# Kernel optimization log

Measured on AMD Instinct MI355X. Metric: run time of the kernel, lower is better.

Reference implementation:

```python
import jax, jax.numpy as jnp
import numpy as np

NUM_HEADS = 16
HIDDEN = 1024
HEAD_DIM = HIDDEN // NUM_HEADS
LN_EPS = 1e-5


def setup_inputs() -> dict:
    key = jax.random.key(0)
    ks = jax.random.split(key, 10)
    B, S, D = 2, 2048, HIDDEN
    std = 1.0 / np.sqrt(D)
    inp = {
        "hidden_states": jax.random.normal(ks[0], (B, S, D), dtype=jnp.float32),
        "attention_mask": jnp.zeros((B, 1, 1, S), dtype=jnp.float32),
        "Wq": jax.random.normal(ks[1], (D, D), dtype=jnp.float32) * std,
        "bq": jnp.zeros((D,), dtype=jnp.float32),
        "Wk": jax.random.normal(ks[2], (D, D), dtype=jnp.float32) * std,
        "bk": jnp.zeros((D,), dtype=jnp.float32),
        "Wv": jax.random.normal(ks[3], (D, D), dtype=jnp.float32) * std,
        "bv": jnp.zeros((D,), dtype=jnp.float32),
        "Wo": jax.random.normal(ks[4], (D, D), dtype=jnp.float32) * std,
        "bo": jnpp if False else jnp.zeros((D,), dtype=jnp.float32),
        "ln_gamma": jnp.ones((D,), dtype=jnp.float32),
        "ln_beta": jnp.zeros((D,), dtype=jnp.float32),
    }
    return inp


def _mha(x, mask, Wq, bq, Wk, bk, Wv, bv, Wo, bo, ln_gamma, ln_beta):
    B, S, D = x.shape
    H, Hd = NUM_HEADS, HEAD_DIM
    scale = 1.0 / np.sqrt(Hd).astype(np.float32)

    def split_heads(t):  # [B,S,D] -> [B,H,S,Hd]
        return t.reshape(B, S, H, Hd).transpose(0, 2, 1, 3)

    q = split_heads(x @ Wq + bq)
    k = split_heads(x @ Wk + bk)
    v = split_heads(x @ Wv + bv)

    scores = jnp.einsum("bhqd,bhkd->bhqk", q, k) * scale + mask
    probs = jax.nn.softmax(scores, axis=-1)
    ctx = jnp.einsum("bhqk,bhkd->bhqd", probs, v)
    ctx = ctx.transpose(0, 2, 1, 3).reshape(B, S, D)

    out = ctx @ Wo + bo
    resid = out + x
    mu = jnp.mean(resid, axis=-1, keepdims=True)
    var = jnp.var(resid, axis=-1, keepdims=True)
    return (resid - mu) * jax.lax.rsqrt(var + LN_EPS) * ln_gamma + ln_beta


def reference(hidden_states, attention_mask, Wq, bq, Wk, bk, Wv, bv, Wo, bo, ln_gamma, ln_beta):
    return _mha(hidden_states, attention_mask, Wq, bq, Wk, bk, Wv, bv, Wo, bo, ln_gamma, ln_beta)
```

## Files before the change

kernel.cpp:

```cpp
#include <hip/hip_runtime.h>
#include <hip/hip_bf16.h>
#include <stdint.h>

#define NUMH 16
#define HD   64
#define HID  1024
#define SEQ  2048
#define BATCH 2
#define NTOK (BATCH*SEQ)
#define LN_EPS 1e-5f

typedef __attribute__((ext_vector_type(8)))  short  short8;
typedef __attribute__((ext_vector_type(4)))  float  f32x4;
typedef __attribute__((ext_vector_type(16))) float  f32x16;

#define AS1 __attribute__((address_space(1)))
#define AS3 __attribute__((address_space(3)))

__device__ __forceinline__ void gload_lds16(const void* g, void* l) {
  __builtin_amdgcn_global_load_lds((const AS1 void*)g, (AS3 void*)l, 16, 0, 0);
}

__device__ __forceinline__ unsigned short f2bf(float f) {
  union { float f; unsigned u; } v; v.f = f;
  unsigned u = v.u;
  u += 0x7fffu + ((u >> 16) & 1u);
  return (unsigned short)(u >> 16);
}

__device__ __forceinline__ f32x4 mfma16x16x32(short8 a, short8 b, f32x4 c) {
  return __builtin_amdgcn_mfma_f32_16x16x32_bf16(a, b, c, 0, 0, 0);
}
__device__ __forceinline__ f32x16 mfma32x32x16(short8 a, short8 b, f32x16 c) {
  return __builtin_amdgcn_mfma_f32_32x32x16_bf16(a, b, c, 0, 0, 0);
}

__device__ __forceinline__ unsigned cvtpk(float lo, float hi) {
  unsigned r;
  asm("v_cvt_pk_bf16_f32 %0, %1, %2" : "=v"(r) : "v"(lo), "v"(hi));
  return r;
}
__device__ __forceinline__ void perm32swap(unsigned &a, unsigned &b) {
  asm volatile("v_permlane32_swap_b32 %0, %1" : "+v"(a), "+v"(b));
}
__device__ __forceinline__ float xhalf_max(float x) {
  union { float f; unsigned u; } a, b; a.f = x; b.f = x;
  perm32swap(a.u, b.u);
  return fmaxf(a.f, b.f);
}
__device__ __forceinline__ float xhalf_sum(float x) {
  union { float f; unsigned u; } a, b; a.f = x; b.f = x;
  perm32swap(a.u, b.u);
  return a.f + b.f;
}

__global__ void k_conv_x(const float* __restrict__ x, unsigned short* __restrict__ xb) {
  int i = blockIdx.x * blockDim.x + threadIdx.x;
  f32x4 v = ((const f32x4*)x)[i];
  unsigned short* o = xb + i * 4;
  o[0] = f2bf(v[0]); o[1] = f2bf(v[1]); o[2] = f2bf(v[2]); o[3] = f2bf(v[3]);
}

__global__ void k_transw_all(const float* __restrict__ Wq, const float* __restrict__ Wk,
                             const float* __restrict__ Wv, const float* __restrict__ Wo,
                             unsigned short* __restrict__ WqkvT, unsigned short* __restrict__ WoT) {
  __shared__ float t[32][33];
  int z = blockIdx.z;
  const float* in = (z == 0) ? Wq : (z == 1) ? Wk : (z == 2) ? Wv : Wo;
  unsigned short* out = (z < 3) ? WqkvT + (size_t)z * HID * HID : WoT;
  int tx = threadIdx.x, ty = threadIdx.y;
  int x0 = blockIdx.x * 32, y0 = blockIdx.y * 32;
  for (int j = 0; j < 32; j += 8)
    t[ty + j][tx] = in[(y0 + ty + j) * HID + x0 + tx];
  __syncthreads();
  for (int j = 0; j < 32; j += 8)
    out[(x0 + ty + j) * HID + y0 + tx] = f2bf(t[tx][ty + j]);
}

template<int MODE>
__global__ __launch_bounds__(256, 2)
void k_gemm(const unsigned short* __restrict__ A, const unsigned short* __restrict__ BT,
            int M, int N, int K,
            const float* __restrict__ bias0, const float* __restrict__ bias1,
            const float* __restrict__ bias2, const float* __restrict__ resid,
            unsigned short* __restrict__ outQ, unsigned short* __restrict__ outK,
            unsigned short* __restrict__ outV, float* __restrict__ outF) {
  const int tid  = threadIdx.x;
  const int lane = tid & 63, wave = tid >> 6;
  const int l15 = lane & 15, lhi = lane >> 4;
  const int row0 = blockIdx.x * 128, col0 = blockIdx.y * 128;
  const int wrow = (wave >> 1) * 64, wcol = (wave & 1) * 64;

  __shared__ unsigned short As[128 * 32];
  __shared__ unsigned short Bs[128 * 32];

  f32x4 acc[4][4] = {};

  for (int kt = 0; kt < K; kt += 32) {
    #pragma unroll
    for (int c = 0; c < 2; ++c) {
      int base = wave * 1024 + c * 4096;
      int o = base + lane * 16;
      int r = o >> 6, cb = o & 63;
      gload_lds16(A  + (size_t)(row0 + r) * K + kt + (cb >> 1), As + (base >> 1));
      gload_lds16(BT + (size_t)(col0 + r) * K + kt + (cb >> 1), Bs + (base >> 1));
    }
    __syncthreads();

    short8 af[4], bf[4];
    #pragma unroll
    for (int m = 0; m < 4; ++m)
      af[m] = *(const short8*)(As + (wrow + m * 16 + l15) * 32 + lhi * 8);
    #pragma unroll
    for (int n = 0; n < 4; ++n)
      bf[n] = *(const short8*)(Bs + (wcol + n * 16 + l15) * 32 + lhi * 8);
    #pragma unroll
    for (int m = 0; m < 4; ++m)
      #pragma unroll
      for (int n = 0; n < 4; ++n)
        acc[m][n] = mfma16x16x32(af[m], bf[n], acc[m][n]);
    __syncthreads();
  }

  #pragma unroll
  for (int m = 0; m < 4; ++m)
    #pragma unroll
    for (int n = 0; n < 4; ++n) {
      int col = col0 + wcol + n * 16 + l15;
      #pragma unroll
      for (int j = 0; j < 4; ++j) {
        int row = row0 + wrow + m * 16 + lhi * 4 + j;
        float v = acc[m][n][j];
        if (MODE == 0) {
          int proj = col >> 10, d = col & 1023;
          int h = d >> 6, hd = d & 63;
          int b = row >> 11, s = row & 2047;
          const float* bias = (proj == 0) ? bias0 : (proj == 1) ? bias1 : bias2;
          unsigned short* dst = (proj == 0) ? outQ : (proj == 1) ? outK : outV;
          dst[((size_t)((b * NUMH + h) * SEQ + s) << 6) + hd] = f2bf(v + bias[d]);
        } else {
          size_t idx = (size_t)row * N + col;
          outF[idx] = v + bias0[col] + resid[idx];
        }
      }
    }
}

__global__ void k_vtrans(const unsigned short* __restrict__ V, unsigned short* __restrict__ VT) {
  __shared__ unsigned short t[64][65];
  int bh = blockIdx.y, s0 = blockIdx.x * 64;
  int tid = threadIdx.x;
  for (int it = 0; it < 16; ++it) {
    int idx = it * 256 + tid;
    int r = idx >> 6, c = idx & 63;
    t[r][c] = V[(size_t)(bh * SEQ + s0 + r) * 64 + c];
  }
  __syncthreads();
  for (int it = 0; it < 16; ++it) {
    int idx = it * 256 + tid;
    int d = idx >> 6, sl = idx & 63;
    VT[(size_t)(bh * 64 + d) * SEQ + s0 + sl] = t[sl][d];
  }
}

__global__ __launch_bounds__(256, 2)
void k_attn(const unsigned short* __restrict__ Q, const unsigned short* __restrict__ Kk,
            const unsigned short* __restrict__ VT, const float* __restrict__ mask,
            unsigned short* __restrict__ ctx) {
  const int tid = threadIdx.x, lane = tid & 63, wave = tid >> 6;
  const int l31 = lane & 31, hi = lane >> 5;
  const int bh = blockIdx.x, b = bh >> 4, h = bh & 15;
  const int qs = blockIdx.y * 128 + wave * 32;

  __shared__ __align__(16) unsigned short Ks[2][64 * 64];
  __shared__ __align__(16) unsigned short Vs[2][64 * 64];
  __shared__ __align__(16) float sLds[4][32];

  short8 qf[4];
  {
    const unsigned short* qrow = Q + ((size_t)bh * SEQ + qs + l31) * 64 + hi * 8;
    #pragma unroll
    for (int ks = 0; ks < 4; ++ks) qf[ks] = *(const short8*)(qrow + ks * 16);
  }

  f32x16 o0 = {}, o1 = {};
  float mr = -3.0e38f, lr = 0.f;
  const float LOG2E = 1.44269504088896340736f;
  const float scale = 0.125f;
  const int sw = (l31 & 7) << 4;

  auto stage = [&](int bufi, int kt) {
    #pragma unroll
    for (int c = 0; c < 2; ++c) {
      int base = wave * 1024 + c * 4096;
      int off = base + lane * 16;
      int r = off >> 7, cb = off & 127;
      int scb = cb ^ ((r & 7) << 4);
      gload_lds16(Kk + ((size_t)bh * SEQ + kt + r) * 64 + (scb >> 1), &Ks[bufi][base >> 1]);
      gload_lds16(VT + ((size_t)bh * 64 + r) * SEQ + kt + (scb >> 1), &Vs[bufi][base >> 1]);
    }
  };

  stage(0, 0);
  __syncthreads();
  int cur = 0;

  for (int kt = 0; kt < SEQ; kt += 64) {
    if (kt + 64 < SEQ) stage(cur ^ 1, kt + 64);

    const unsigned short* Kc = Ks[cur];
    const unsigned short* Vc = Vs[cur];
    f32x16 s0 = {}, s1 = {};
    #pragma unroll
    for (int ks = 0; ks < 4; ++ks) {
      int cb = ((ks * 16 + hi * 8) * 2) ^ sw;
      short8 k0 = *(const short8*)((const char*)Kc + l31 * 128 + cb);
      short8 k1 = *(const short8*)((const char*)Kc + (32 + l31) * 128 + cb);
      s0 = mfma32x32x16(k0, qf[ks], s0);
      s1 = mfma32x32x16(k1, qf[ks], s1);
    }

    f32x4 mk0[4], mk1[4];
    #pragma unroll
    for (int rq = 0; rq < 4; ++rq) {
      mk0[rq] = *(const f32x4*)(mask + b * SEQ + kt + rq * 8 + hi * 4);
      mk1[rq] = *(const f32x4*)(mask + b * SEQ + kt + 32 + rq * 8 + hi * 4);
    }
    #pragma unroll
    for (int r = 0; r < 16; ++r) {
      s0[r] = fmaf(s0[r], scale, mk0[r >> 2][r & 3]);
      s1[r] = fmaf(s1[r], scale, mk1[r >> 2][r & 3]);
    }

    float tmax = fmaxf(s0[0], s1[0]);
    #pragma unroll
    for (int r = 1; r < 16; ++r) tmax = fmaxf(tmax, fmaxf(s0[r], s1[r]));
    tmax = xhalf_max(tmax);

    if (!__all(tmax <= mr + 8.0f)) {
      float mnew = fmaxf(mr, tmax);
      float alpha = exp2f((mr - mnew) * LOG2E);
      mr = mnew; lr *= alpha;
      if (hi == 0) sLds[wave][l31] = alpha;
      f32x4 av[4];
      #pragma unroll
      for (int rq = 0; rq < 4; ++rq) av[rq] = *(const f32x4*)&sLds[wave][rq * 8 + hi * 4];
      #pragma unroll
      for (int r = 0; r < 16; ++r) {
        o0[r] *= av[r >> 2][r & 3];
        o1[r] *= av[r >> 2][r & 3];
      }
    }

    float mL = mr * LOG2E;
    float rs = 0.f;
    #pragma unroll
    for (int r = 0; r < 16; ++r) {
      float p0 = exp2f(fmaf(s0[r], LOG2E, -mL));
      float p1 = exp2f(fmaf(s1[r], LOG2E, -mL));
      s0[r] = p0; s1[r] = p1; rs += p0 + p1;
    }
    lr += xhalf_sum(rs);

    unsigned pw[4][4];
    #pragma unroll
    for (int ks = 0; ks < 4; ++ks) {
      int ro = 8 * (ks & 1);
      unsigned a0, a1, b0, b1;
      if (ks < 2) {
        a0 = cvtpk(s0[ro + 0], s0[ro + 1]); a1 = cvtpk(s0[ro + 2], s0[ro + 3]);
        b0 = cvtpk(s0[ro + 4], s0[ro + 5]); b1 = cvtpk(s0[ro + 6], s0[ro + 7]);
      } else {
        a0 = cvtpk(s1[ro + 0], s1[ro + 1]); a1 = cvtpk(s1[ro + 2], s1[ro + 3]);
        b0 = cvtpk(s1[ro + 4], s1[ro + 5]); b1 = cvtpk(s1[ro + 6], s1[ro + 7]);
      }
      perm32swap(a0, b0);
      perm32swap(a1, b1);
      pw[ks][0] = a0; pw[ks][1] = a1; pw[ks][2] = b0; pw[ks][3] = b1;
    }

    #pragma unroll
    for (int ks = 0; ks < 4; ++ks) {
      union { unsigned u[4]; short8 s; } pu;
      pu.u[0] = pw[ks][0]; pu.u[1] = pw[ks][1]; pu.u[2] = pw[ks][2]; pu.u[3] = pw[ks][3];
      int cb = ((ks * 16 + hi * 8) * 2) ^ sw;
      short8 v0 = *(const short8*)((const char*)Vc + l31 * 128 + cb);
      short8 v1 = *(const short8*)((const char*)Vc + (32 + l31) * 128 + cb);
      o0 = mfma32x32x16(pu.s, v0, o0);
      o1 = mfma32x32x16(pu.s, v1, o1);
    }

    __syncthreads();
    cur ^= 1;
  }

  if (hi == 0) sLds[wave][l31] = lr;
  f32x4 lv[4];
  #pragma unroll
  for (int rq = 0; rq < 4; ++rq) {
    f32x4 t = *(const f32x4*)&sLds[wave][rq * 8 + hi * 4];
    lv[rq][0] = 1.f / t[0]; lv[rq][1] = 1.f / t[1];
    lv[rq][2] = 1.f / t[2]; lv[rq][3] = 1.f / t[3];
  }
  #pragma unroll
  for (int r = 0; r < 16; ++r) {
    int q = qs + (r & 3) + 8 * (r >> 2) + 4 * hi;
    float inv = lv[r >> 2][r & 3];
    unsigned short* dst = ctx + (size_t)(b * SEQ + q) * HID + h * 64;
    dst[l31]      = f2bf(o0[r] * inv);
    dst[32 + l31] = f2bf(o1[r] * inv);
  }
}

__global__ __launch_bounds__(256)
void k_ln(const float* __restrict__ resid, const float* __restrict__ gamma,
          const float* __restrict__ beta, float* __restrict__ out) {
  int row = blockIdx.x, tid = threadIdx.x;
  f32x4 v = ((const f32x4*)(resid + (size_t)row * HID))[tid];
  float s = v[0] + v[1] + v[2] + v[3];
  float ss = v[0]*v[0] + v[1]*v[1] + v[2]*v[2] + v[3]*v[3];
  #pragma unroll
  for (int off = 1; off < 64; off <<= 1) { s += __shfl_xor(s, off); ss += __shfl_xor(ss, off); }
  __shared__ float sb[4], ssb[4];
  int wave = tid >> 6, lane = tid & 63;
  if (lane == 0) { sb[wave] = s; ssb[wave] = ss; }
  __syncthreads();
  float ts = sb[0] + sb[1] + sb[2] + sb[3];
  float tss = ssb[0] + ssb[1] + ssb[2] + ssb[3];
  float mu = ts * (1.f / HID);
  float var = tss * (1.f / HID) - mu * mu;
  float rstd = rsqrtf(var + LN_EPS);
  f32x4 g = ((const f32x4*)gamma)[tid];
  f32x4 be = ((const f32x4*)beta)[tid];
  f32x4 o;
  #pragma unroll
  for (int i = 0; i < 4; ++i) o[i] = (v[i] - mu) * rstd * g[i] + be[i];
  ((f32x4*)(out + (size_t)row * HID))[tid] = o;
}

extern "C" void kernel_launch(void* const* d_in, const int* in_sizes, int n_in,
                              void* d_out, int out_size, void* d_ws, size_t ws_size,
                              hipStream_t stream) {
  const float* x     = (const float*)d_in[0];
  const float* mask  = (const float*)d_in[1];
  const float* Wq    = (const float*)d_in[2];
  const float* bq    = (const float*)d_in[3];
  const float* Wk    = (const float*)d_in[4];
  const float* bk    = (const float*)d_in[5];
  const float* Wv    = (const float*)d_in[6];
  const float* bv    = (const float*)d_in[7];
  const float* Wo    = (const float*)d_in[8];
  const float* bo    = (const float*)d_in[9];
  const float* gamma = (const float*)d_in[10];
  const float* beta  = (const float*)d_in[11];
  float* out = (float*)d_out;

  char* w = (char*)d_ws;
  unsigned short* xb    = (unsigned short*)w; w += (size_t)NTOK * HID * 2;
  unsigned short* WqkvT = (unsigned short*)w; w += (size_t)3 * HID * HID * 2;
  unsigned short* WoT   = (unsigned short*)w; w += (size_t)HID * HID * 2;
  unsigned short* Qh    = (unsigned short*)w; w += (size_t)NTOK * HID * 2;
  unsigned short* Kh    = (unsigned short*)w; w += (size_t)NTOK * HID * 2;
  unsigned short* Vh    = (unsigned short*)w; w += (size_t)NTOK * HID * 2;
  unsigned short* VTh   = (unsigned short*)w; w += (size_t)NTOK * HID * 2;
  unsigned short* ctxb  = (unsigned short*)w; w += (size_t)NTOK * HID * 2;
  float*          attn  = (float*)w;          w += (size_t)NTOK * HID * 4;
  (void)ws_size; (void)in_sizes; (void)n_in; (void)out_size;

  k_conv_x<<<NTOK * HID / 4 / 256, 256, 0, stream>>>(x, xb);
  k_transw_all<<<dim3(32, 32, 4), dim3(32, 8), 0, stream>>>(Wq, Wk, Wv, Wo, WqkvT, WoT);

  k_gemm<0><<<dim3(NTOK / 128, 3 * HID / 128), 256, 0, stream>>>(
      xb, WqkvT, NTOK, 3 * HID, HID, bq, bk, bv, nullptr, Qh, Kh, Vh, nullptr);

  k_vtrans<<<dim3(SEQ / 64, BATCH * NUMH), 256, 0, stream>>>(Vh, VTh);

  k_attn<<<dim3(BATCH * NUMH, SEQ / 128), 256, 0, stream>>>(Qh, Kh, VTh, mask, ctxb);

  k_gemm<1><<<dim3(NTOK / 128, HID / 128), 256, 0, stream>>>(
      ctxb, WoT, NTOK, HID, HID, bo, nullptr, nullptr, x, nullptr, nullptr, nullptr, attn);

  k_ln<<<NTOK, 256, 0, stream>>>(attn, gamma, beta, out);
}
```

Before: 233.8 us.

## Double K-tile depth in GEMM and KV block size in attention, add setprio

The GEMM now stages 64-wide K slices instead of 32, which halves the number of barrier-separated iterations. The attention kernel processes 128 keys per iteration instead of 64, with a 16-row XOR swizzle for the wider V tile. The MFMA sections are wrapped in s_setprio to favour matrix issue. The cost is more LDS per block (64KB K/V double buffer in attention) and more live registers, which may lower occupancy.

```diff
diff --git a/kernel.cpp b/kernel.cpp
--- a/kernel.cpp
+++ b/kernel.cpp
@@ -91,34 +91,37 @@
   const int row0 = blockIdx.x * 128, col0 = blockIdx.y * 128;
   const int wrow = (wave >> 1) * 64, wcol = (wave & 1) * 64;
 
-  __shared__ unsigned short As[128 * 32];
-  __shared__ unsigned short Bs[128 * 32];
+  __shared__ unsigned short As[128 * 64];
+  __shared__ unsigned short Bs[128 * 64];
 
   f32x4 acc[4][4] = {};
 
-  for (int kt = 0; kt < K; kt += 32) {
-    #pragma unroll
-    for (int c = 0; c < 2; ++c) {
+  for (int kt = 0; kt < K; kt += 64) {
+    #pragma unroll
+    for (int c = 0; c < 4; ++c) {
       int base = wave * 1024 + c * 4096;
       int o = base + lane * 16;
-      int r = o >> 6, cb = o & 63;
+      int r = o >> 7, cb = o & 127;
       gload_lds16(A  + (size_t)(row0 + r) * K + kt + (cb >> 1), As + (base >> 1));
       gload_lds16(BT + (size_t)(col0 + r) * K + kt + (cb >> 1), Bs + (base >> 1));
     }
     __syncthreads();
 
-    short8 af[4], bf[4];
-    #pragma unroll
-    for (int m = 0; m < 4; ++m)
-      af[m] = *(const short8*)(As + (wrow + m * 16 + l15) * 32 + lhi * 8);
-    #pragma unroll
-    for (int n = 0; n < 4; ++n)
-      bf[n] = *(const short8*)(Bs + (wcol + n * 16 + l15) * 32 + lhi * 8);
-    #pragma unroll
-    for (int m = 0; m < 4; ++m)
+    #pragma unroll
+    for (int kk = 0; kk < 2; ++kk) {
+      short8 af[4], bf[4];
+      #pragma unroll
+      for (int m = 0; m < 4; ++m)
+        af[m] = *(const short8*)(As + (wrow + m * 16 + l15) * 64 + kk * 32 + lhi * 8);
       #pragma unroll
       for (int n = 0; n < 4; ++n)
-        acc[m][n] = mfma16x16x32(af[m], bf[n], acc[m][n]);
+        bf[n] = *(const short8*)(Bs + (wcol + n * 16 + l15) * 64 + kk * 32 + lhi * 8);
+      #pragma unroll
+      for (int m = 0; m < 4; ++m)
+        #pragma unroll
+        for (int n = 0; n < 4; ++n)
+          acc[m][n] = mfma16x16x32(af[m], bf[n], acc[m][n]);
+    }
     __syncthreads();
   }
 
@@ -172,8 +175,8 @@
   const int bh = blockIdx.x, b = bh >> 4, h = bh & 15;
   const int qs = blockIdx.y * 128 + wave * 32;
 
-  __shared__ __align__(16) unsigned short Ks[2][64 * 64];
-  __shared__ __align__(16) unsigned short Vs[2][64 * 64];
+  __shared__ __align__(16) unsigned short Ks[2][128 * 64];
+  __shared__ __align__(16) unsigned short Vs[2][64 * 128];
   __shared__ __align__(16) float sLds[4][32];
 
   short8 qf[4];
@@ -187,17 +190,20 @@
   float mr = -3.0e38f, lr = 0.f;
   const float LOG2E = 1.44269504088896340736f;
   const float scale = 0.125f;
-  const int sw = (l31 & 7) << 4;
+  const int swK = (l31 & 7) << 4;
+  const int swV = (l31 & 15) << 4;
 
   auto stage = [&](int bufi, int kt) {
     #pragma unroll
-    for (int c = 0; c < 2; ++c) {
+    for (int c = 0; c < 4; ++c) {
       int base = wave * 1024 + c * 4096;
       int off = base + lane * 16;
-      int r = off >> 7, cb = off & 127;
-      int scb = cb ^ ((r & 7) << 4);
-      gload_lds16(Kk + ((size_t)bh * SEQ + kt + r) * 64 + (scb >> 1), &Ks[bufi][base >> 1]);
-      gload_lds16(VT + ((size_t)bh * 64 + r) * SEQ + kt + (scb >> 1), &Vs[bufi][base >> 1]);
+      int rk = off >> 7, cbk = off & 127;
+      int sk = cbk ^ ((rk & 7) << 4);
+      gload_lds16(Kk + ((size_t)bh * SEQ + kt + rk) * 64 + (sk >> 1), &Ks[bufi][base >> 1]);
+      int rv = off >> 8, cbv = off & 255;
+      int sv = cbv ^ ((rv & 15) << 4);
+      gload_lds16(VT + ((size_t)bh * 64 + rv) * SEQ + kt + (sv >> 1), &Vs[bufi][base >> 1]);
     }
   };
 
@@ -205,36 +211,40 @@
   __syncthreads();
   int cur = 0;
 
-  for (int kt = 0; kt < SEQ; kt += 64) {
-    if (kt + 64 < SEQ) stage(cur ^ 1, kt + 64);
-
-    const unsigned short* Kc = Ks[cur];
-    const unsigned short* Vc = Vs[cur];
-    f32x16 s0 = {}, s1 = {};
-    #pragma unroll
-    for (int ks = 0; ks < 4; ++ks) {
-      int cb = ((ks * 16 + hi * 8) * 2) ^ sw;
-      short8 k0 = *(const short8*)((const char*)Kc + l31 * 128 + cb);
-      short8 k1 = *(const short8*)((const char*)Kc + (32 + l31) * 128 + cb);
-      s0 = mfma32x32x16(k0, qf[ks], s0);
-      s1 = mfma32x32x16(k1, qf[ks], s1);
-    }
-
-    f32x4 mk0[4], mk1[4];
-    #pragma unroll
-    for (int rq = 0; rq < 4; ++rq) {
-      mk0[rq] = *(const f32x4*)(mask + b * SEQ + kt + rq * 8 + hi * 4);
-      mk1[rq] = *(const f32x4*)(mask + b * SEQ + kt + 32 + rq * 8 + hi * 4);
-    }
-    #pragma unroll
-    for (int r = 0; r < 16; ++r) {
-      s0[r] = fmaf(s0[r], scale, mk0[r >> 2][r & 3]);
-      s1[r] = fmaf(s1[r], scale, mk1[r >> 2][r & 3]);
-    }
-
-    float tmax = fmaxf(s0[0], s1[0]);
-    #pragma unroll
-    for (int r = 1; r < 16; ++r) tmax = fmaxf(tmax, fmaxf(s0[r], s1[r]));
+  for (int kt = 0; kt < SEQ; kt += 128) {
+    if (kt + 128 < SEQ) stage(cur ^ 1, kt + 128);
+
+    const char* Kc = (const char*)Ks[cur];
+    const char* Vc = (const char*)Vs[cur];
+
+    f32x16 s[4] = {};
+    __builtin_amdgcn_s_setprio(1);
+    #pragma unroll
+    for (int kb = 0; kb < 4; ++kb)
+      #pragma unroll
+      for (int ks = 0; ks < 4; ++ks) {
+        int cb = ((ks * 16 + hi * 8) * 2) ^ swK;
+        short8 kf = *(const short8*)(Kc + (kb * 32 + l31) * 128 + cb);
+        s[kb] = mfma32x32x16(kf, qf[ks], s[kb]);
+      }
+    __builtin_amdgcn_s_setprio(0);
+
+    #pragma unroll
+    for (int kb = 0; kb < 4; ++kb) {
+      f32x4 mk[4];
+      #pragma unroll
+      for (int rq = 0; rq < 4; ++rq)
+        mk[rq] = *(const f32x4*)(mask + b * SEQ + kt + kb * 32 + rq * 8 + hi * 4);
+      #pragma unroll
+      for (int r = 0; r < 16; ++r)
+        s[kb][r] = fmaf(s[kb][r], scale, mk[r >> 2][r & 3]);
+    }
+
+    float tmax = s[0][0];
+    #pragma unroll
+    for (int kb = 0; kb < 4; ++kb)
+      #pragma unroll
+      for (int r = 0; r < 16; ++r) tmax = fmaxf(tmax, s[kb][r]);
     tmax = xhalf_max(tmax);
 
     if (!__all(tmax <= mr + 8.0f)) {
@@ -255,40 +265,42 @@
     float mL = mr * LOG2E;
     float rs = 0.f;
     #pragma unroll
-    for (int r = 0; r < 16; ++r) {
-      float p0 = exp2f(fmaf(s0[r], LOG2E, -mL));
-      float p1 = exp2f(fmaf(s1[r], LOG2E, -mL));
-      s0[r] = p0; s1[r] = p1; rs += p0 + p1;
-    }
+    for (int kb = 0; kb < 4; ++kb)
+      #pragma unroll
+      for (int r = 0; r < 16; ++r) {
+        float p = exp2f(fmaf(s[kb][r], LOG2E, -mL));
+        s[kb][r] = p; rs += p;
+      }
     lr += xhalf_sum(rs);
 
-    unsigned pw[4][4];
-    #pragma unroll
-    for (int ks = 0; ks < 4; ++ks) {
-      int ro = 8 * (ks & 1);
-      unsigned a0, a1, b0, b1;
-      if (ks < 2) {
-        a0 = cvtpk(s0[ro + 0], s0[ro + 1]); a1 = cvtpk(s0[ro + 2], s0[ro + 3]);
-        b0 = cvtpk(s0[ro + 4], s0[ro + 5]); b1 = cvtpk(s0[ro + 6], s0[ro + 7]);
-      } else {
-        a0 = cvtpk(s1[ro + 0], s1[ro + 1]); a1 = cvtpk(s1[ro + 2], s1[ro + 3]);
-        b0 = cvtpk(s1[ro + 4], s1[ro + 5]); b1 = cvtpk(s1[ro + 6], s1[ro + 7]);
-      }
-      perm32swap(a0, b0);
-      perm32swap(a1, b1);
-      pw[ks][0] = a0; pw[ks][1] = a1; pw[ks][2] = b0; pw[ks][3] = b1;
-    }
-
-    #pragma unroll
-    for (int ks = 0; ks < 4; ++ks) {
-      union { unsigned u[4]; short8 s; } pu;
-      pu.u[0] = pw[ks][0]; pu.u[1] = pw[ks][1]; pu.u[2] = pw[ks][2]; pu.u[3] = pw[ks][3];
-      int cb = ((ks * 16 + hi * 8) * 2) ^ sw;
-      short8 v0 = *(const short8*)((const char*)Vc + l31 * 128 + cb);
-      short8 v1 = *(const short8*)((const char*)Vc + (32 + l31) * 128 + cb);
-      o0 = mfma32x32x16(pu.s, v0, o0);
-      o1 = mfma32x32x16(pu.s, v1, o1);
-    }
+    unsigned pw[8][4];
+    #pragma unroll
+    for (int kb = 0; kb < 4; ++kb)
+      #pragma unroll
+      for (int k2 = 0; k2 < 2; ++k2) {
+        int ro = 8 * k2;
+        unsigned a0 = cvtpk(s[kb][ro + 0], s[kb][ro + 1]);
+        unsigned a1 = cvtpk(s[kb][ro + 2], s[kb][ro + 3]);
+        unsigned b0 = cvtpk(s[kb][ro + 4], s[kb][ro + 5]);
+        unsigned b1 = cvtpk(s[kb][ro + 6], s[kb][ro + 7]);
+        perm32swap(a0, b0);
+        perm32swap(a1, b1);
+        pw[kb * 2 + k2][0] = a0; pw[kb * 2 + k2][1] = a1;
+        pw[kb * 2 + k2][2] = b0; pw[kb * 2 + k2][3] = b1;
+      }
+
+    __builtin_amdgcn_s_setprio(1);
+    #pragma unroll
+    for (int sl = 0; sl < 8; ++sl) {
+      union { unsigned u[4]; short8 s8; } pu;
+      pu.u[0] = pw[sl][0]; pu.u[1] = pw[sl][1]; pu.u[2] = pw[sl][2]; pu.u[3] = pw[sl][3];
+      int cb = ((sl * 16 + hi * 8) * 2) ^ swV;
+      short8 v0 = *(const short8*)(Vc + l31 * 256 + cb);
+      short8 v1 = *(const short8*)(Vc + (32 + l31) * 256 + cb);
+      o0 = mfma32x32x16(pu.s8, v0, o0);
+      o1 = mfma32x32x16(pu.s8, v1, o1);
+    }
+    __builtin_amdgcn_s_setprio(0);
 
     __syncthreads();
     cur ^= 1;
```

Measured after the change: 238.1 us. No clear change (+1.8%).
